# Optimization experiments

Hardware: AMD Instinct MI355X
Metric: run time of the kernel (lower is better)

The kernel has to match this reference:

```python
import jax, jax.numpy as jnp
import numpy as np

VOCAB, HDIM, NCLS, NLEAF = 32000, 128, 5, 65536


def _lin(key, fan_in, fan_out):
    kw, kb = jax.random.split(key)
    s = 1.0 / np.sqrt(fan_in)
    W = jax.random.uniform(kw, (fan_in, fan_out), jnp.float32, -s, s)
    b = jax.random.uniform(kb, (fan_out,), jnp.float32, -s, s)
    return W, b


def setup_inputs() -> dict:
    key = jax.random.key(0)
    ks = jax.random.split(key, 11)
    words = jax.random.randint(ks[0], (NLEAF,), 0, VOCAB, dtype=jnp.int64)
    emb = jax.random.normal(ks[1], (VOCAB, HDIM), jnp.float32)
    Wi, bi = _lin(ks[2], HDIM, HDIM)
    Wo, bo = _lin(ks[3], HDIM, HDIM)
    Wu, bu = _lin(ks[4], HDIM, HDIM)
    Ui, bUi = _lin(ks[5], 2 * HDIM, HDIM)
    Uo, bUo = _lin(ks[6], 2 * HDIM, HDIM)
    Uu, bUu = _lin(ks[7], 2 * HDIM, HDIM)
    Uf1, bf1 = _lin(ks[8], HDIM, HDIM)
    Uf2, bf2 = _lin(ks[9], HDIM, HDIM)
    P, bP = _lin(ks[10], HDIM, NCLS)
    return dict(words=words, emb=emb, Wi=Wi, bi=bi, Wo=Wo, bo=bo, Wu=Wu, bu=bu,
                Ui=Ui, bUi=bUi, Uo=Uo, bUo=bUo, Uu=Uu, bUu=bUu,
                Uf1=Uf1, bf1=bf1, Uf2=Uf2, bf2=bf2, P=P, bP=bP)


def reference(words, emb, Wi, bi, Wo, bo, Wu, bu, Ui, bUi, Uo, bUo, Uu, bUu,
              Uf1, bf1, Uf2, bf2, P, bP):
    sig = jax.nn.sigmoid
    # Leaf cells: batch all leaves at once.
    e = emb[words]                                  # [L, h]
    i = sig(e @ Wi + bi)
    o = sig(e @ Wo + bo)
    u = jax.nn.relu(e @ Wu + bu)
    c = i * u
    h = o * jax.nn.relu(c)
    all_h = [h]
    # Perfect binary tree: internal node j at each level combines
    # children (2j, 2j+1) of the previous level -> batch each level.
    while h.shape[0] > 1:
        lH, rH = h[0::2], h[1::2]
        lC, rC = c[0::2], c[1::2]
        eN = jnp.concatenate([lH, rH], axis=-1)     # [n/2, 2h]
        i = sig(eN @ Ui + bUi)
        o = sig(eN @ Uo + bUo)
        u = jax.nn.relu(eN @ Uu + bUu)
        c = i * u + sig(lH @ Uf1 + bf1) * lC + sig(rH @ Uf2 + bf2) * rC
        h = o * jax.nn.relu(c)
        all_h.append(h)
    H = jnp.concatenate(all_h, axis=0)              # [2L-1, h], leaves-first level order
    return H @ P + bP                               # per-node class logits
```

## Files before the change

### kernel.cpp

```cpp
#include <hip/hip_runtime.h>
#include <cstdint>
#include <cstddef>

#define NCLS 5

typedef unsigned short ushort_t;
typedef __attribute__((ext_vector_type(8))) short short8v;
typedef __attribute__((ext_vector_type(4))) float f32x4;

__device__ __forceinline__ float sigf(float x) { return 1.0f / (1.0f + __expf(-x)); }

__device__ __forceinline__ unsigned short bf16_rne(float x) {
    unsigned u = __float_as_uint(x);
    u += 0x7FFFu + ((u >> 16) & 1u);
    return (unsigned short)(u >> 16);
}
__device__ __forceinline__ float bf16_f32(unsigned short h) {
    return __uint_as_float(((unsigned)h) << 16);
}

__device__ __forceinline__ void cvt_hilo(float4 f0, float4 f1, short8v& hi, short8v& lo) {
    float v[8] = { f0.x, f0.y, f0.z, f0.w, f1.x, f1.y, f1.z, f1.w };
#pragma unroll
    for (int e = 0; e < 8; ++e) {
        unsigned short h = bf16_rne(v[e]);
        unsigned short l = bf16_rne(v[e] - bf16_f32(h));
        hi[e] = (short)h; lo[e] = (short)l;
    }
}

__global__ __launch_bounds__(256)
void prep_w(const float* __restrict__ Wi, const float* __restrict__ Wo,
            const float* __restrict__ Wu,
            const float* __restrict__ Ui, const float* __restrict__ Uo,
            const float* __restrict__ Uu, const float* __restrict__ Uf1,
            const float* __restrict__ Uf2, const float* __restrict__ P,
            ushort_t* __restrict__ WtPL, ushort_t* __restrict__ WtPF,
            ushort_t* __restrict__ PT)
{
    int b = blockIdx.x;
    if (b < 1024) {
        int idx = b * 256 + threadIdx.x;
        int e = idx & 7, lane = (idx >> 3) & 63;
        int slot = (idx >> 9) & 3, cc = (idx >> 11) & 15, cb = idx >> 15;
        int j  = cb * 16 + (lane & 15);
        int kq = (lane >> 4) * 8 + e;
        int band = cc >> 3, c8 = cc & 7, csel = c8 >> 2;
        int kc = (c8 & 3) * 32 + kq;
        float x;
        if      (slot == 0) x = Ui[(csel * 128 + kc) * 128 + j];
        else if (slot == 1) x = Uo[(csel * 128 + kc) * 128 + j];
        else if (slot == 2) x = Uu[(csel * 128 + kc) * 128 + j];
        else                x = csel ? Uf2[kc * 128 + j] : Uf1[kc * 128 + j];
        unsigned short h = bf16_rne(x);
        if (band) h = bf16_rne(x - bf16_f32(h));
        WtPL[idx] = h;
    } else if (b < 1408) {
        int idx = (b - 1024) * 256 + threadIdx.x;
        if (idx >= 98304) return;
        int e = idx & 7, lane = (idx >> 3) & 63;
        int rest = idx >> 9;
        int slot = rest % 3, cc = (rest / 3) & 7, cb = rest / 24;
        int j  = cb * 16 + (lane & 15);
        int kq = (lane >> 4) * 8 + e;
        int band = cc >> 2;
        int kc = (cc & 3) * 32 + kq;
        const float* W = (slot == 0) ? Wi : (slot == 1) ? Wo : Wu;
        float x = W[kc * 128 + j];
        unsigned short h = bf16_rne(x);
        if (band) h = bf16_rne(x - bf16_f32(h));
        WtPF[idx] = h;
    } else {
        int idx = (b - 1408) * 256 + threadIdx.x;
        if (idx >= 4096) return;
        int e = idx & 7, lane = (idx >> 3) & 63, cc = idx >> 9;
        int col = lane & 15;
        int kq  = (lane >> 4) * 8 + e;
        int band = cc >> 2;
        int kc = (cc & 3) * 32 + kq;
        float x = (col < NCLS) ? P[kc * NCLS + col] : 0.f;
        unsigned short h = bf16_rne(x);
        if (band) h = bf16_rne(x - bf16_f32(h));
        PT[idx] = h;
    }
}

__global__ __launch_bounds__(512)
void leaf_stream(const int* __restrict__ words, const float* __restrict__ emb,
                 const ushort_t* __restrict__ WtPF,
                 const float* __restrict__ bi, const float* __restrict__ bo,
                 const float* __restrict__ bu,
                 ushort_t* __restrict__ H2out, ushort_t* __restrict__ C2out)
{
    __shared__ ushort_t EA[32 * 264];
    const int tid = threadIdx.x, lane = tid & 63, wc = tid >> 6;
    const int l15 = lane & 15, l4 = lane >> 4;
    const int rb = blockIdx.x * 32;
    const ushort_t* slab = WtPF + (size_t)wc * 12288;

    {
        const int rl = wc * 4 + (lane >> 4);
        const int g  = lane & 15;
        const float* e = emb + (size_t)words[rb + rl] * 128 + g * 8;
        float4 f0 = *(const float4*)(e);
        float4 f1 = *(const float4*)(e + 4);
        short8v hi, lo;
        cvt_hilo(f0, f1, hi, lo);
        *(short8v*)(EA + rl * 264 + g * 8)       = hi;
        *(short8v*)(EA + rl * 264 + 128 + g * 8) = lo;
    }
    __syncthreads();

    f32x4 acc[2][3];
#pragma unroll
    for (int fr = 0; fr < 2; ++fr)
#pragma unroll
        for (int g = 0; g < 3; ++g) acc[fr][g] = (f32x4){0.f, 0.f, 0.f, 0.f};

    short8v pB0, pB1, pB2, pB3, pB4, pB5;
#define LEAF_B(c) do {                                                        \
        pB0 = *(const short8v*)(slab + (size_t)((c) * 3 + 0) * 512 + lane * 8); \
        pB1 = *(const short8v*)(slab + (size_t)((c) * 3 + 1) * 512 + lane * 8); \
        pB2 = *(const short8v*)(slab + (size_t)((c) * 3 + 2) * 512 + lane * 8); \
        pB3 = *(const short8v*)(slab + (size_t)(((c) + 4) * 3 + 0) * 512 + lane * 8); \
        pB4 = *(const short8v*)(slab + (size_t)(((c) + 4) * 3 + 1) * 512 + lane * 8); \
        pB5 = *(const short8v*)(slab + (size_t)(((c) + 4) * 3 + 2) * 512 + lane * 8); \
    } while (0)

    LEAF_B(0);
#pragma unroll
    for (int cc = 0; cc < 4; ++cc) {
        short8v Bh[3] = { pB0, pB1, pB2 };
        short8v Bl[3] = { pB3, pB4, pB5 };
        if (cc < 3) LEAF_B(cc + 1);
        const int ko = cc * 32 + l4 * 8;
        short8v Ah0 = *(const short8v*)(EA + l15 * 264 + ko);
        short8v Ah1 = *(const short8v*)(EA + (16 + l15) * 264 + ko);
        short8v Al0 = *(const short8v*)(EA + l15 * 264 + 128 + ko);
        short8v Al1 = *(const short8v*)(EA + (16 + l15) * 264 + 128 + ko);
#pragma unroll
        for (int s = 0; s < 3; ++s) {
            acc[0][s] = __builtin_amdgcn_mfma_f32_16x16x32_bf16(Ah0, Bh[s], acc[0][s], 0, 0, 0);
            acc[1][s] = __builtin_amdgcn_mfma_f32_16x16x32_bf16(Ah1, Bh[s], acc[1][s], 0, 0, 0);
            acc[0][s] = __builtin_amdgcn_mfma_f32_16x16x32_bf16(Al0, Bh[s], acc[0][s], 0, 0, 0);
            acc[1][s] = __builtin_amdgcn_mfma_f32_16x16x32_bf16(Al1, Bh[s], acc[1][s], 0, 0, 0);
            acc[0][s] = __builtin_amdgcn_mfma_f32_16x16x32_bf16(Ah0, Bl[s], acc[0][s], 0, 0, 0);
            acc[1][s] = __builtin_amdgcn_mfma_f32_16x16x32_bf16(Ah1, Bl[s], acc[1][s], 0, 0, 0);
        }
    }
#undef LEAF_B

    const int j = wc * 16 + l15;
    const float bi_ = bi[j], bo_ = bo[j], bu_ = bu[j];
#pragma unroll
    for (int fr = 0; fr < 2; ++fr)
#pragma unroll
        for (int v = 0; v < 4; ++v) {
            const int row = rb + fr * 16 + l4 * 4 + v;
            float iv = sigf(acc[fr][0][v] + bi_);
            float ov = sigf(acc[fr][1][v] + bo_);
            float uv = fmaxf(acc[fr][2][v] + bu_, 0.f);
            float c_ = iv * uv;
            float h_ = ov * fmaxf(c_, 0.f);
            unsigned short chi = bf16_rne(c_);
            unsigned short clo = bf16_rne(c_ - bf16_f32(chi));
            unsigned short hhi = bf16_rne(h_);
            unsigned short hlo = bf16_rne(h_ - bf16_f32(hhi));
            C2out[(size_t)row * 256 + j]       = chi;
            C2out[(size_t)row * 256 + 128 + j] = clo;
            H2out[(size_t)row * 256 + j]       = hhi;
            H2out[(size_t)row * 256 + 128 + j] = hlo;
        }
}

__global__ __launch_bounds__(512)
void level_lds(const ushort_t* __restrict__ H2in, const ushort_t* __restrict__ C2in,
               const ushort_t* __restrict__ WtPL,
               const float* __restrict__ bUi, const float* __restrict__ bUo,
               const float* __restrict__ bUu, const float* __restrict__ bf1,
               const float* __restrict__ bf2,
               ushort_t* __restrict__ H2out, ushort_t* __restrict__ C2out)
{
    __shared__ ushort_t EA[64 * 264];
    const int tid = threadIdx.x, lane = tid & 63, wc = tid >> 6;
    const int l15 = lane & 15, l4 = lane >> 4;
    const int rb = blockIdx.x * 32;
    const ushort_t* slab = WtPL + (size_t)wc * 32768;

    {
        const ushort_t* src = H2in + (size_t)(2 * rb) * 256;
        const int cr  = tid >> 3;
        const int seg = tid & 7;
#pragma unroll
        for (int i = 0; i < 4; ++i) {
            short8v v = *(const short8v*)(src + cr * 256 + seg * 32 + i * 8);
            *(short8v*)(EA + cr * 264 + seg * 32 + i * 8) = v;
        }
    }
    __syncthreads();

    f32x4 acc[2][5];
#pragma unroll
    for (int fr = 0; fr < 2; ++fr)
#pragma unroll
        for (int g = 0; g < 5; ++g) acc[fr][g] = (f32x4){0.f, 0.f, 0.f, 0.f};

#pragma unroll
    for (int cc = 0; cc < 8; ++cc) {
        const int csel = cc >> 2;
        const int ko = (cc & 3) * 32 + l4 * 8;
        short8v Ah0 = *(const short8v*)(EA + (2 * l15 + csel) * 264 + ko);
        short8v Ah1 = *(const short8v*)(EA + (2 * (16 + l15) + csel) * 264 + ko);
        short8v Al0 = *(const short8v*)(EA + (2 * l15 + csel) * 264 + 128 + ko);
        short8v Al1 = *(const short8v*)(EA + (2 * (16 + l15) + csel) * 264 + 128 + ko);
        short8v Bh[4], Bw[4];
#pragma unroll
        for (int s = 0; s < 4; ++s) {
            Bh[s] = *(const short8v*)(slab + (size_t)(cc * 4 + s) * 512 + lane * 8);
            Bw[s] = *(const short8v*)(slab + (size_t)((cc + 8) * 4 + s) * 512 + lane * 8);
        }
#pragma unroll
        for (int s = 0; s < 4; ++s) {
            const int col = (s < 3) ? s : 3 + csel;
            acc[0][col] = __builtin_amdgcn_mfma_f32_16x16x32_bf16(Ah0, Bh[s], acc[0][col], 0, 0, 0);
            acc[1][col] = __builtin_amdgcn_mfma_f32_16x16x32_bf16(Ah1, Bh[s], acc[1][col], 0, 0, 0);
            acc[0][col] = __builtin_amdgcn_mfma_f32_16x16x32_bf16(Al0, Bh[s], acc[0][col], 0, 0, 0);
            acc[1][col] = __builtin_amdgcn_mfma_f32_16x16x32_bf16(Al1, Bh[s], acc[1][col], 0, 0, 0);
            acc[0][col] = __builtin_amdgcn_mfma_f32_16x16x32_bf16(Ah0, Bw[s], acc[0][col], 0, 0, 0);
            acc[1][col] = __builtin_amdgcn_mfma_f32_16x16x32_bf16(Ah1, Bw[s], acc[1][col], 0, 0, 0);
        }
    }

    const int j = wc * 16 + l15;
    const float b0_ = bUi[j], b1_ = bUo[j], b2_ = bUu[j], b3_ = bf1[j], b4_ = bf2[j];
#pragma unroll
    for (int fr = 0; fr < 2; ++fr)
#pragma unroll
        for (int v = 0; v < 4; ++v) {
            const int row = rb + fr * 16 + l4 * 4 + v;
            float iv  = sigf(acc[fr][0][v] + b0_);
            float ov  = sigf(acc[fr][1][v] + b1_);
            float uv  = fmaxf(acc[fr][2][v] + b2_, 0.f);
            float f1v = sigf(acc[fr][3][v] + b3_);
            float f2v = sigf(acc[fr][4][v] + b4_);
            const ushort_t* cl = C2in + (size_t)(2 * row) * 256;
            float lC = bf16_f32(cl[j])       + bf16_f32(cl[128 + j]);
            float rC = bf16_f32(cl[256 + j]) + bf16_f32(cl[384 + j]);
            float c_ = fmaf(iv, uv, fmaf(f1v, lC, f2v * rC));
            float h_ = ov * fmaxf(c_, 0.f);
            unsigned short chi = bf16_rne(c_);
            unsigned short clo = bf16_rne(c_ - bf16_f32(chi));
            unsigned short hhi = bf16_rne(h_);
            unsigned short hlo = bf16_rne(h_ - bf16_f32(hhi));
            C2out[(size_t)row * 256 + j]       = chi;
            C2out[(size_t)row * 256 + 128 + j] = clo;
            H2out[(size_t)row * 256 + j]       = hhi;
            H2out[(size_t)row * 256 + 128 + j] = hlo;
        }
}

__global__ __launch_bounds__(64)
void level_tiny(const ushort_t* __restrict__ H2in, const ushort_t* __restrict__ C2in,
                const ushort_t* __restrict__ WtPL,
                const float* __restrict__ bUi, const float* __restrict__ bUo,
                const float* __restrict__ bUu, const float* __restrict__ bf1,
                const float* __restrict__ bf2,
                ushort_t* __restrict__ H2out, ushort_t* __restrict__ C2out, int n)
{
    const int lane = threadIdx.x;
    const int l15 = lane & 15, l4 = lane >> 4;
    const int cb = blockIdx.y;
    const int rb = blockIdx.x * 16;
    const ushort_t* slab = WtPL + (size_t)cb * 32768;

    int prow = rb + l15; if (prow > n - 1) prow = n - 1;
    const ushort_t* r0 = H2in + (size_t)(2 * prow) * 256;

    f32x4 acc[5];
#pragma unroll
    for (int g = 0; g < 5; ++g) acc[g] = (f32x4){0.f, 0.f, 0.f, 0.f};

#pragma unroll
    for (int cc = 0; cc < 8; ++cc) {
        const int csel = cc >> 2;
        const int aoff = csel * 256 + (cc & 3) * 32 + l4 * 8;
        short8v Ah = *(const short8v*)(r0 + aoff);
        short8v Al = *(const short8v*)(r0 + aoff + 128);
#pragma unroll
        for (int s = 0; s < 4; ++s) {
            const int col = (s < 3) ? s : 3 + csel;
            short8v Bh = *(const short8v*)(slab + (size_t)(cc * 4 + s) * 512 + lane * 8);
            short8v Bw = *(const short8v*)(slab + (size_t)((cc + 8) * 4 + s) * 512 + lane * 8);
            acc[col] = __builtin_amdgcn_mfma_f32_16x16x32_bf16(Ah, Bh, acc[col], 0, 0, 0);
            acc[col] = __builtin_amdgcn_mfma_f32_16x16x32_bf16(Al, Bh, acc[col], 0, 0, 0);
            acc[col] = __builtin_amdgcn_mfma_f32_16x16x32_bf16(Ah, Bw, acc[col], 0, 0, 0);
        }
    }

    const int j = cb * 16 + l15;
    const float b0_ = bUi[j], b1_ = bUo[j], b2_ = bUu[j], b3_ = bf1[j], b4_ = bf2[j];
#pragma unroll
    for (int v = 0; v < 4; ++v) {
        const int row = rb + l4 * 4 + v;
        if (row < n) {
            float iv  = sigf(acc[0][v] + b0_);
            float ov  = sigf(acc[1][v] + b1_);
            float uv  = fmaxf(acc[2][v] + b2_, 0.f);
            float f1v = sigf(acc[3][v] + b3_);
            float f2v = sigf(acc[4][v] + b4_);
            const ushort_t* cl = C2in + (size_t)(2 * row) * 256;
            float lC = bf16_f32(cl[j])       + bf16_f32(cl[128 + j]);
            float rC = bf16_f32(cl[256 + j]) + bf16_f32(cl[384 + j]);
            float c_ = fmaf(iv, uv, fmaf(f1v, lC, f2v * rC));
            float h_ = ov * fmaxf(c_, 0.f);
            unsigned short chi = bf16_rne(c_);
            unsigned short clo = bf16_rne(c_ - bf16_f32(chi));
            unsigned short hhi = bf16_rne(h_);
            unsigned short hlo = bf16_rne(h_ - bf16_f32(hhi));
            C2out[(size_t)row * 256 + j]       = chi;
            C2out[(size_t)row * 256 + 128 + j] = clo;
            H2out[(size_t)row * 256 + j]       = hhi;
            H2out[(size_t)row * 256 + 128 + j] = hlo;
        }
    }
}

__global__ __launch_bounds__(256)
void proj_mfma(const ushort_t* __restrict__ H2, const ushort_t* __restrict__ PT,
               const float* __restrict__ bP, float* __restrict__ out, int total)
{
    const int tid = threadIdx.x, lane = tid & 63, w = tid >> 6;
    const int l15 = lane & 15, l4 = lane >> 4;
    const int rb = (blockIdx.x * 4 + w) * 16;

    int ar = rb + l15; if (ar > total - 1) ar = total - 1;
    const ushort_t* hr = H2 + (size_t)ar * 256;

    f32x4 acc = (f32x4){0.f, 0.f, 0.f, 0.f};
#pragma unroll
    for (int cc = 0; cc < 4; ++cc) {
        const int ko = cc * 32 + l4 * 8;
        short8v Ah = *(const short8v*)(hr + ko);
        short8v Al = *(const short8v*)(hr + 128 + ko);
        short8v Bh = *(const short8v*)(PT + ((size_t)(cc * 64) + lane) * 8);
        short8v Bl = *(const short8v*)(PT + ((size_t)((cc + 4) * 64) + lane) * 8);
        acc = __builtin_amdgcn_mfma_f32_16x16x32_bf16(Ah, Bh, acc, 0, 0, 0);
        acc = __builtin_amdgcn_mfma_f32_16x16x32_bf16(Al, Bh, acc, 0, 0, 0);
        acc = __builtin_amdgcn_mfma_f32_16x16x32_bf16(Ah, Bl, acc, 0, 0, 0);
    }

    if (l15 < NCLS) {
        const float b = bP[l15];
#pragma unroll
        for (int v = 0; v < 4; ++v) {
            const int row = rb + l4 * 4 + v;
            if (row < total)
                out[(size_t)row * NCLS + l15] = acc[v] + b;
        }
    }
}

extern "C" void kernel_launch(void* const* d_in, const int* in_sizes, int n_in,
                              void* d_out, int out_size, void* d_ws, size_t ws_size,
                              hipStream_t stream)
{
    const int*   words = (const int*)  d_in[0];
    const float* emb   = (const float*)d_in[1];
    const float* Wi  = (const float*)d_in[2];  const float* bi  = (const float*)d_in[3];
    const float* Wo  = (const float*)d_in[4];  const float* bo  = (const float*)d_in[5];
    const float* Wu  = (const float*)d_in[6];  const float* bu  = (const float*)d_in[7];
    const float* Ui  = (const float*)d_in[8];  const float* bUi = (const float*)d_in[9];
    const float* Uo  = (const float*)d_in[10]; const float* bUo = (const float*)d_in[11];
    const float* Uu  = (const float*)d_in[12]; const float* bUu = (const float*)d_in[13];
    const float* Uf1 = (const float*)d_in[14]; const float* bf1 = (const float*)d_in[15];
    const float* Uf2 = (const float*)d_in[16]; const float* bf2 = (const float*)d_in[17];
    const float* Pm  = (const float*)d_in[18]; const float* bP  = (const float*)d_in[19];
    float* out = (float*)d_out;

    ushort_t* WtPL = (ushort_t*)d_ws;
    ushort_t* WtPF = (ushort_t*)((char*)d_ws + 524288);
    ushort_t* PT   = (ushort_t*)((char*)d_ws + 720896);
    ushort_t* H2   = (ushort_t*)((char*)d_ws + 1048576);
    ushort_t* C2   = (ushort_t*)((char*)d_ws + 68157440);

    prep_w<<<1424, 256, 0, stream>>>(Wi, Wo, Wu, Ui, Uo, Uu, Uf1, Uf2, Pm,
                                     WtPL, WtPF, PT);

    leaf_stream<<<2048, 512, 0, stream>>>(words, emb, WtPF, bi, bo, bu, H2, C2);

    int off_prev = 0, off = 65536, m = 32768;
    while (m >= 8192) {
        level_lds<<<m / 32, 512, 0, stream>>>(
            H2 + (size_t)off_prev * 256, C2 + (size_t)off_prev * 256, WtPL,
            bUi, bUo, bUu, bf1, bf2,
            H2 + (size_t)off * 256, C2 + (size_t)off * 256);
        off_prev = off; off += m; m >>= 1;
    }

    while (m >= 1) {
        level_tiny<<<dim3((m + 15) / 16, 8), 64, 0, stream>>>(
            H2 + (size_t)off_prev * 256, C2 + (size_t)off_prev * 256, WtPL,
            bUi, bUo, bUu, bf1, bf2,
            H2 + (size_t)off * 256, C2 + (size_t)off * 256, m);
        off_prev = off; off += m; m >>= 1;
    }

    proj_mfma<<<2048, 256, 0, stream>>>(H2, PT, bP, out, 131071);
}
```

Baseline: 214.8 us.

## Fuse pairs of small tree levels into one kernel via shared-memory handoff

Adds a tail2 kernel that computes two consecutive tree levels in one launch. The first level's h/c results for a 16-row tile go to LDS, and the next level's 8 parents are computed from that tile. This replaces the per-level level_tiny launches for levels 4096 down to 2, roughly halving kernel launches and the global round trips between small levels. In exchange, the second phase uses only half the MFMA rows, and the grid is smaller than before for the first level of each pair.

```diff
diff --git a/kernel.cpp b/kernel.cpp
--- a/kernel.cpp
+++ b/kernel.cpp
@@ -259,6 +259,138 @@
         }
 }
 
+__global__ __launch_bounds__(512)
+void tail2(const ushort_t* __restrict__ H2in, const ushort_t* __restrict__ C2in,
+           const ushort_t* __restrict__ WtPL,
+           const float* __restrict__ bUi, const float* __restrict__ bUo,
+           const float* __restrict__ bUu, const float* __restrict__ bf1,
+           const float* __restrict__ bf2,
+           ushort_t* __restrict__ H2A, ushort_t* __restrict__ C2A,
+           ushort_t* __restrict__ H2B, ushort_t* __restrict__ C2B, int mA)
+{
+    __shared__ ushort_t Hl[16 * 264];
+    __shared__ ushort_t Cl[16 * 264];
+    const int tid = threadIdx.x, lane = tid & 63, wc = tid >> 6;
+    const int l15 = lane & 15, l4 = lane >> 4;
+    const ushort_t* slab = WtPL + (size_t)wc * 32768;
+    const int j = wc * 16 + l15;
+    const float b0_ = bUi[j], b1_ = bUo[j], b2_ = bUu[j], b3_ = bf1[j], b4_ = bf2[j];
+    const int rbA = blockIdx.x * 16;
+
+    {
+        int prow = rbA + l15; if (prow > mA - 1) prow = mA - 1;
+        const ushort_t* r0 = H2in + (size_t)(2 * prow) * 256;
+
+        f32x4 acc[5];
+#pragma unroll
+        for (int g = 0; g < 5; ++g) acc[g] = (f32x4){0.f, 0.f, 0.f, 0.f};
+
+#pragma unroll
+        for (int cc = 0; cc < 8; ++cc) {
+            const int csel = cc >> 2;
+            const int aoff = csel * 256 + (cc & 3) * 32 + l4 * 8;
+            short8v Ah = *(const short8v*)(r0 + aoff);
+            short8v Al = *(const short8v*)(r0 + aoff + 128);
+#pragma unroll
+            for (int s = 0; s < 4; ++s) {
+                const int col = (s < 3) ? s : 3 + csel;
+                short8v Bh = *(const short8v*)(slab + (size_t)(cc * 4 + s) * 512 + lane * 8);
+                short8v Bw = *(const short8v*)(slab + (size_t)((cc + 8) * 4 + s) * 512 + lane * 8);
+                acc[col] = __builtin_amdgcn_mfma_f32_16x16x32_bf16(Ah, Bh, acc[col], 0, 0, 0);
+                acc[col] = __builtin_amdgcn_mfma_f32_16x16x32_bf16(Al, Bh, acc[col], 0, 0, 0);
+                acc[col] = __builtin_amdgcn_mfma_f32_16x16x32_bf16(Ah, Bw, acc[col], 0, 0, 0);
+            }
+        }
+
+#pragma unroll
+        for (int v = 0; v < 4; ++v) {
+            const int lr = l4 * 4 + v;
+            const int row = rbA + lr;
+            if (row < mA) {
+                float iv  = sigf(acc[0][v] + b0_);
+                float ov  = sigf(acc[1][v] + b1_);
+                float uv  = fmaxf(acc[2][v] + b2_, 0.f);
+                float f1v = sigf(acc[3][v] + b3_);
+                float f2v = sigf(acc[4][v] + b4_);
+                const ushort_t* cl = C2in + (size_t)(2 * row) * 256;
+                float lC = bf16_f32(cl[j])       + bf16_f32(cl[128 + j]);
+                float rC = bf16_f32(cl[256 + j]) + bf16_f32(cl[384 + j]);
+                float c_ = fmaf(iv, uv, fmaf(f1v, lC, f2v * rC));
+                float h_ = ov * fmaxf(c_, 0.f);
+                unsigned short chi = bf16_rne(c_);
+                unsigned short clo = bf16_rne(c_ - bf16_f32(chi));
+                unsigned short hhi = bf16_rne(h_);
+                unsigned short hlo = bf16_rne(h_ - bf16_f32(hhi));
+                C2A[(size_t)row * 256 + j]       = chi;
+                C2A[(size_t)row * 256 + 128 + j] = clo;
+                H2A[(size_t)row * 256 + j]       = hhi;
+                H2A[(size_t)row * 256 + 128 + j] = hlo;
+                Hl[lr * 264 + j]       = hhi;
+                Hl[lr * 264 + 128 + j] = hlo;
+                Cl[lr * 264 + j]       = chi;
+                Cl[lr * 264 + 128 + j] = clo;
+            }
+        }
+    }
+    __syncthreads();
+
+    {
+        const int mB = mA >> 1;
+        const int rbB = blockIdx.x * 8;
+        int lp = (l15 > 7) ? 7 : l15;
+        if (rbB + lp > mB - 1) lp = (mB - 1) - rbB;
+
+        f32x4 acc[5];
+#pragma unroll
+        for (int g = 0; g < 5; ++g) acc[g] = (f32x4){0.f, 0.f, 0.f, 0.f};
+
+#pragma unroll
+        for (int cc = 0; cc < 8; ++cc) {
+            const int csel = cc >> 2;
+            const int ko = (cc & 3) * 32 + l4 * 8;
+            const ushort_t* ra = Hl + (size_t)(2 * lp + csel) * 264;
+            short8v Ah = *(const short8v*)(ra + ko);
+            short8v Al = *(const short8v*)(ra + 128 + ko);
+#pragma unroll
+            for (int s = 0; s < 4; ++s) {
+                const int col = (s < 3) ? s : 3 + csel;
+                short8v Bh = *(const short8v*)(slab + (size_t)(cc * 4 + s) * 512 + lane * 8);
+                short8v Bw = *(const short8v*)(slab + (size_t)((cc + 8) * 4 + s) * 512 + lane * 8);
+                acc[col] = __builtin_amdgcn_mfma_f32_16x16x32_bf16(Ah, Bh, acc[col], 0, 0, 0);
+                acc[col] = __builtin_amdgcn_mfma_f32_16x16x32_bf16(Al, Bh, acc[col], 0, 0, 0);
+                acc[col] = __builtin_amdgcn_mfma_f32_16x16x32_bf16(Ah, Bw, acc[col], 0, 0, 0);
+            }
+        }
+
+#pragma unroll
+        for (int v = 0; v < 4; ++v) {
+            const int lr = l4 * 4 + v;
+            const int row = rbB + lr;
+            if (lr < 8 && row < mB) {
+                float iv  = sigf(acc[0][v] + b0_);
+                float ov  = sigf(acc[1][v] + b1_);
+                float uv  = fmaxf(acc[2][v] + b2_, 0.f);
+                float f1v = sigf(acc[3][v] + b3_);
+                float f2v = sigf(acc[4][v] + b4_);
+                float lC = bf16_f32(Cl[(2 * lr) * 264 + j])
+                         + bf16_f32(Cl[(2 * lr) * 264 + 128 + j]);
+                float rC = bf16_f32(Cl[(2 * lr + 1) * 264 + j])
+                         + bf16_f32(Cl[(2 * lr + 1) * 264 + 128 + j]);
+                float c_ = fmaf(iv, uv, fmaf(f1v, lC, f2v * rC));
+                float h_ = ov * fmaxf(c_, 0.f);
+                unsigned short chi = bf16_rne(c_);
+                unsigned short clo = bf16_rne(c_ - bf16_f32(chi));
+                unsigned short hhi = bf16_rne(h_);
+                unsigned short hlo = bf16_rne(h_ - bf16_f32(hhi));
+                C2B[(size_t)row * 256 + j]       = chi;
+                C2B[(size_t)row * 256 + 128 + j] = clo;
+                H2B[(size_t)row * 256 + j]       = hhi;
+                H2B[(size_t)row * 256 + 128 + j] = hlo;
+            }
+        }
+    }
+}
+
 __global__ __launch_bounds__(64)
 void level_tiny(const ushort_t* __restrict__ H2in, const ushort_t* __restrict__ C2in,
                 const ushort_t* __restrict__ WtPL,
@@ -397,13 +529,25 @@
         off_prev = off; off += m; m >>= 1;
     }
 
-    while (m >= 1) {
-        level_tiny<<<dim3((m + 15) / 16, 8), 64, 0, stream>>>(
+    int mA = 4096;
+    while (mA >= 4) {
+        int offA = off;
+        int offB = off + mA;
+        int grid = (mA >= 16) ? (mA / 16) : 1;
+        tail2<<<grid, 512, 0, stream>>>(
             H2 + (size_t)off_prev * 256, C2 + (size_t)off_prev * 256, WtPL,
             bUi, bUo, bUu, bf1, bf2,
-            H2 + (size_t)off * 256, C2 + (size_t)off * 256, m);
-        off_prev = off; off += m; m >>= 1;
-    }
+            H2 + (size_t)offA * 256, C2 + (size_t)offA * 256,
+            H2 + (size_t)offB * 256, C2 + (size_t)offB * 256, mA);
+        off_prev = offB;
+        off = offB + (mA >> 1);
+        mA >>= 2;
+    }
+
+    level_tiny<<<dim3(1, 8), 64, 0, stream>>>(
+        H2 + (size_t)off_prev * 256, C2 + (size_t)off_prev * 256, WtPL,
+        bUi, bUo, bUu, bf1, bf2,
+        H2 + (size_t)off * 256, C2 + (size_t)off * 256, 1);
 
     proj_mfma<<<2048, 256, 0, stream>>>(H2, PT, bP, out, 131071);
 }
```

Measured after the change: 233.0 us. 8.5% more time.
